# Performance work log

Measured on AMD Instinct MI355X. Metric: run time of the kernel, lower is better.

Reference implementation:

```python
import jax, jax.numpy as jnp
import numpy as np

N_NODES = 100000
N_EDGES = 1600000
D_IN = 64
D_OUT = 64
NUM_ETYPE = 2
NEG_SLOPE = 0.2


def setup_inputs() -> dict:
    key = jax.random.key(0)
    ks = jax.random.split(key, 9)
    feat = jax.random.normal(ks[0], (N_NODES, D_IN), dtype=jnp.float32)
    rel = jax.random.uniform(ks[1], (N_EDGES, NUM_ETYPE), dtype=jnp.float32)
    W_self = jax.random.normal(ks[2], (D_OUT, D_IN), dtype=jnp.float32) * 0.1
    b_self = jax.random.normal(ks[3], (D_OUT,), dtype=jnp.float32) * 0.1
    W_neigh = jax.random.normal(ks[4], (D_OUT, D_IN), dtype=jnp.float32) * 0.1
    b_neigh = jax.random.normal(ks[5], (D_OUT,), dtype=jnp.float32) * 0.1
    attn_e = jax.random.normal(ks[6], (NUM_ETYPE, 1), dtype=jnp.float32)
    src = jax.random.randint(ks[7], (N_EDGES,), 0, N_NODES, dtype=jnp.int32)
    dst = jax.random.randint(ks[8], (N_EDGES,), 0, N_NODES, dtype=jnp.int32)
    return {"feat": feat, "rel": rel, "W_self": W_self, "b_self": b_self,
            "W_neigh": W_neigh, "b_neigh": b_neigh, "attn_e": attn_e,
            "src": src, "dst": dst}


def reference(feat, rel, W_self, b_self, W_neigh, b_neigh, attn_e, src, dst):
    n = feat.shape[0]
    # per-edge attention score: [E, num_etype] @ [num_etype, 1] -> [E]
    e = jnp.squeeze(rel @ attn_e, axis=1)
    e = jax.nn.leaky_relu(e, negative_slope=NEG_SLOPE)
    # edge_softmax: segment softmax over edges grouped by destination node
    emax = jax.ops.segment_max(e, dst, num_segments=n)          # [N]
    ex = jnp.exp(e - emax[dst])                                  # [E]
    denom = jax.ops.segment_sum(ex, dst, num_segments=n)        # [N]
    a = ex / denom[dst]                                          # [E]
    # u_mul_e + sum aggregation: neigh[v] = sum_e a_e * feat[src_e]
    m = feat[src] * a[:, None]                                   # [E, D_IN]
    h_neigh = jax.ops.segment_sum(m, dst, num_segments=n)       # [N, D_IN]
    # rst = fc_self(h_self) + fc_neigh(h_neigh)  (torch Linear: x @ W.T + b)
    return feat @ W_self.T + b_self + h_neigh @ W_neigh.T + b_neigh
```

## Files before the change

kernel.cpp:

```cpp
#include <hip/hip_runtime.h>
#include <hip/hip_bf16.h>

#define N_NODES 100000
#define N_EDGES 1600000
#define D 64
#define NEG_SLOPE 0.2f

#define BSHIFT 10
#define BNODES 1024
#define NBUCK ((N_NODES + BNODES - 1) >> BSHIFT)
#define BUCKET_CAP 17408
#define P1_EPB 4096
#define P1_T 512
#define P1_IT (P1_EPB / P1_T)

__global__ __launch_bounds__(P1_T) void binning_kernel(
    const float2* __restrict__ rel, const float* __restrict__ attn_e,
    const int* __restrict__ src, const int* __restrict__ dst,
    int* __restrict__ bucket_cursor, uint2* __restrict__ binned)
{
    __shared__ uint2 staged1[P1_EPB];
    __shared__ uint2 staged2[P1_EPB];
    __shared__ int cnt[NBUCK];
    __shared__ int excl[NBUCK];
    __shared__ int chunkbase[NBUCK];

    int tid = threadIdx.x;
    int e0 = blockIdx.x * P1_EPB;
    int n = min(P1_EPB, N_EDGES - e0);

    for (int b = tid; b < NBUCK; b += P1_T) cnt[b] = 0;
    __syncthreads();

    float a0 = attn_e[0], a1 = attn_e[1];

    int myslot[P1_IT];
    #pragma unroll
    for (int j = 0; j < P1_IT; ++j) {
        int i = tid + j * P1_T;
        if (i < n) {
            int e = e0 + i;
            float2 r = rel[e];
            float sc = r.x * a0 + r.y * a1;
            sc = (sc > 0.f) ? sc : NEG_SLOPE * sc;
            float ev = __expf(sc);
            unsigned u = __float_as_uint(ev) + 0x8000u;
            unsigned wcode = (u >> 16) & 0x7FFFu;
            unsigned s = (unsigned)src[e];
            unsigned d = (unsigned)dst[e];
            staged1[i] = make_uint2((s << 15) | wcode, d);
            myslot[j] = atomicAdd(&cnt[d >> BSHIFT], 1);
        }
    }
    __syncthreads();
    if (tid == 0) {
        int run = 0;
        for (int b = 0; b < NBUCK; ++b) { excl[b] = run; run += cnt[b]; }
    }
    __syncthreads();
    #pragma unroll
    for (int j = 0; j < P1_IT; ++j) {
        int i = tid + j * P1_T;
        if (i < n) {
            uint2 v = staged1[i];
            staged2[excl[v.y >> BSHIFT] + myslot[j]] = v;
        }
    }
    if (tid < NBUCK)
        chunkbase[tid] = atomicAdd(&bucket_cursor[tid], cnt[tid]);
    __syncthreads();
    for (int i = tid; i < n; i += P1_T) {
        uint2 v = staged2[i];
        int b = (int)(v.y >> BSHIFT);
        binned[(size_t)b * BUCKET_CAP + chunkbase[b] + (i - excl[b])] = v;
    }
}

__global__ __launch_bounds__(1024) void csr_kernel(
    const int* __restrict__ bucket_cursor, const uint2* __restrict__ binned,
    int* __restrict__ offsets, unsigned* __restrict__ edata)
{
    __shared__ unsigned vals[BUCKET_CAP];
    __shared__ int hist[BNODES];
    __shared__ int nexcl[BNODES];
    __shared__ int cur[BNODES];
    __shared__ int bc[NBUCK];
    __shared__ int base_sh;

    int b = blockIdx.x;
    int tid = threadIdx.x;

    if (tid < NBUCK) bc[tid] = bucket_cursor[tid];
    hist[tid] = 0;
    cur[tid] = 0;
    __syncthreads();
    if (tid == 0) {
        int s = 0;
        for (int i = 0; i < b; ++i) s += bc[i];
        base_sh = s;
    }
    __syncthreads();
    int count = bc[b];
    int base = base_sh;
    const uint2* bin = binned + (size_t)b * BUCKET_CAP;

    for (int i = tid; i < count; i += 1024)
        atomicAdd(&hist[bin[i].y & (BNODES - 1)], 1);
    __syncthreads();

    int h = hist[tid];
    nexcl[tid] = h;
    __syncthreads();
    for (int d = 1; d < BNODES; d <<= 1) {
        int u = (tid >= d) ? nexcl[tid - d] : 0;
        __syncthreads();
        nexcl[tid] += u;
        __syncthreads();
    }
    int excl = nexcl[tid] - h;
    __syncthreads();
    nexcl[tid] = excl;
    __syncthreads();

    int node = (b << BSHIFT) + tid;
    if (node < N_NODES) offsets[node] = base + excl;
    if (b == NBUCK - 1 && tid == 0) offsets[N_NODES] = N_EDGES;

    for (int i = tid; i < count; i += 1024) {
        uint2 e = bin[i];
        int d = e.y & (BNODES - 1);
        int t = atomicAdd(&cur[d], 1);
        vals[nexcl[d] + t] = e.x;
    }
    __syncthreads();
    for (int i = tid; i < count; i += 1024)
        edata[base + i] = vals[i];
}

__global__ __launch_bounds__(512) void gemm_fused_kernel(
    const float* __restrict__ feat, const float* __restrict__ W_self,
    const float* __restrict__ W_neigh, const float* __restrict__ b_self,
    const float* __restrict__ b_neigh, float* __restrict__ out,
    __hip_bfloat16* __restrict__ g)
{
    __shared__ float Wt[2][D][D + 1];
    __shared__ float fs[64 * D];
    int tid = threadIdx.x;
    #pragma unroll
    for (int i = 0; i < 8; ++i) {
        int idx = tid + i * 512;
        Wt[0][idx & 63][idx >> 6] = W_self[idx];
        Wt[1][idx & 63][idx >> 6] = W_neigh[idx];
    }
    {
        long base4 = (long)blockIdx.x * 1024;
        const float4* f4 = (const float4*)feat;
        float4* s4 = (float4*)fs;
        #pragma unroll
        for (int i = 0; i < 2; ++i) {
            int idx = tid + i * 512;
            if (base4 + idx < (long)N_NODES * D / 4) s4[idx] = f4[base4 + idx];
        }
    }
    __syncthreads();

    int lane = tid & 63;
    int wave = tid >> 6;
    int m = wave >> 2;
    int sw = wave & 3;
    float w[D];
    #pragma unroll
    for (int k = 0; k < D; ++k) w[k] = Wt[m][k][lane];
    float bias = (m == 0) ? (b_self[lane] + b_neigh[lane]) : 0.f;

    int r0 = blockIdx.x * 64 + sw * 16;
    #pragma unroll 1
    for (int rr = 0; rr < 16; ++rr) {
        int r = r0 + rr;
        if (r >= N_NODES) break;
        const float4* frow = (const float4*)(fs + (sw * 16 + rr) * D);
        float acc = 0.f;
        #pragma unroll
        for (int k4 = 0; k4 < 16; ++k4) {
            float4 f = frow[k4];
            acc += f.x * w[4*k4]   + f.y * w[4*k4+1]
                 + f.z * w[4*k4+2] + f.w * w[4*k4+3];
        }
        if (m == 0) out[(size_t)r * D + lane] = acc + bias;
        else        g[(size_t)r * D + lane] = __float2bfloat16(acc);
    }
}

__global__ __launch_bounds__(256) void aggregate_kernel(
    const uint* __restrict__ g32, const unsigned* __restrict__ edata,
    const int* __restrict__ offsets, float* __restrict__ out)
{
    int v = blockIdx.x * 4 + (threadIdx.x >> 6);
    int lane = threadIdx.x & 63;
    int q = lane >> 4;
    int t = lane & 15;
    int lo = offsets[v], hi = offsets[v + 1];
    float4 acc = make_float4(0.f, 0.f, 0.f, 0.f);
    float sum = 0.f;

    for (int i = lo; i < hi; i += 8) {
        int e0 = i + q;
        int e1 = i + 4 + q;
        int ec0 = (e0 < hi) ? e0 : hi - 1;
        int ec1 = (e1 < hi) ? e1 : hi - 1;
        unsigned p0 = edata[ec0];
        unsigned p1 = edata[ec1];
        float w0 = (e0 < hi) ? __uint_as_float((p0 & 0x7FFFu) << 16) : 0.f;
        float w1 = (e1 < hi) ? __uint_as_float((p1 & 0x7FFFu) << 16) : 0.f;
        const uint2* r0 = (const uint2*)(g32 + (size_t)(p0 >> 15) * (D / 2));
        const uint2* r1 = (const uint2*)(g32 + (size_t)(p1 >> 15) * (D / 2));
        uint2 u0 = r0[t];
        uint2 u1 = r1[t];
        acc.x += w0 * __uint_as_float(u0.x << 16);
        acc.y += w0 * __uint_as_float(u0.x & 0xFFFF0000u);
        acc.z += w0 * __uint_as_float(u0.y << 16);
        acc.w += w0 * __uint_as_float(u0.y & 0xFFFF0000u);
        sum += w0;
        acc.x += w1 * __uint_as_float(u1.x << 16);
        acc.y += w1 * __uint_as_float(u1.x & 0xFFFF0000u);
        acc.z += w1 * __uint_as_float(u1.y << 16);
        acc.w += w1 * __uint_as_float(u1.y & 0xFFFF0000u);
        sum += w1;
    }
    #pragma unroll
    for (int mm = 16; mm <= 32; mm <<= 1) {
        acc.x += __shfl_xor(acc.x, mm, 64);
        acc.y += __shfl_xor(acc.y, mm, 64);
        acc.z += __shfl_xor(acc.z, mm, 64);
        acc.w += __shfl_xor(acc.w, mm, 64);
        sum   += __shfl_xor(sum,   mm, 64);
    }
    if (hi > lo && q == 0) {
        float inv = 1.f / sum;
        float4* orow = (float4*)(out + (size_t)v * D);
        float4 c = orow[t];
        c.x += acc.x * inv; c.y += acc.y * inv;
        c.z += acc.z * inv; c.w += acc.w * inv;
        orow[t] = c;
    }
}

extern "C" void kernel_launch(void* const* d_in, const int* in_sizes, int n_in,
                              void* d_out, int out_size, void* d_ws, size_t ws_size,
                              hipStream_t stream) {
    const float* feat    = (const float*)d_in[0];
    const float* rel     = (const float*)d_in[1];
    const float* W_self  = (const float*)d_in[2];
    const float* b_self  = (const float*)d_in[3];
    const float* W_neigh = (const float*)d_in[4];
    const float* b_neigh = (const float*)d_in[5];
    const float* attn_e  = (const float*)d_in[6];
    const int*   src     = (const int*)d_in[7];
    const int*   dst     = (const int*)d_in[8];
    float* out = (float*)d_out;

    uint2* binned = (uint2*)d_ws;
    __hip_bfloat16* g = (__hip_bfloat16*)(binned + (size_t)NBUCK * BUCKET_CAP);
    unsigned* edata = (unsigned*)((char*)g + (size_t)N_NODES * D * 2);
    int* offsets = (int*)(edata + N_EDGES);
    int* bucket_cursor = offsets + N_NODES + 1;

    hipMemsetAsync(bucket_cursor, 0, NBUCK * sizeof(int), stream);

    binning_kernel<<<(N_EDGES + P1_EPB - 1) / P1_EPB, P1_T, 0, stream>>>(
        (const float2*)rel, attn_e, src, dst, bucket_cursor, binned);
    csr_kernel<<<NBUCK, 1024, 0, stream>>>(
        bucket_cursor, binned, offsets, edata);
    gemm_fused_kernel<<<(N_NODES + 63) / 64, 512, 0, stream>>>(
        feat, W_self, W_neigh, b_self, b_neigh, out, g);
    aggregate_kernel<<<N_NODES / 4, 256, 0, stream>>>(
        (const uint*)g, edata, offsets, out);
}
```

Measured before the change: 217.6 us.

## Shrink CSR buckets to 256 nodes, parallelize scans, load GEMM weights directly

Buckets drop from 1024 to 256 nodes each, giving about 391 buckets. The CSR stage therefore gets roughly four times as many blocks, each with 512 threads and smaller shared-memory tiles, which should raise occupancy. The serial single-thread prefix sums over bucket counts in binning and CSR become parallel Hillis-Steele scans, removing a serial bottleneck that now grows with bucket count. The GEMM kernel reads weight rows straight from global memory as float4 instead of transposing them through shared memory, and sets launch bounds to two blocks per CU. The trade-offs are more global atomics and scattered writes per binning block, and a bucket capacity that leaves less headroom for skewed destination distributions.

```diff
diff --git a/kernel.cpp b/kernel.cpp
--- a/kernel.cpp
+++ b/kernel.cpp
@@ -6,10 +6,10 @@
 #define D 64
 #define NEG_SLOPE 0.2f
 
-#define BSHIFT 10
-#define BNODES 1024
+#define BSHIFT 8
+#define BNODES 256
 #define NBUCK ((N_NODES + BNODES - 1) >> BSHIFT)
-#define BUCKET_CAP 17408
+#define BUCKET_CAP 4672
 #define P1_EPB 4096
 #define P1_T 512
 #define P1_IT (P1_EPB / P1_T)
@@ -24,6 +24,7 @@
     __shared__ int cnt[NBUCK];
     __shared__ int excl[NBUCK];
     __shared__ int chunkbase[NBUCK];
+    __shared__ int scanbuf[P1_T];
 
     int tid = threadIdx.x;
     int e0 = blockIdx.x * P1_EPB;
@@ -53,9 +54,17 @@
         }
     }
     __syncthreads();
-    if (tid == 0) {
-        int run = 0;
-        for (int b = 0; b < NBUCK; ++b) { excl[b] = run; run += cnt[b]; }
+    {
+        int c = (tid < NBUCK) ? cnt[tid] : 0;
+        scanbuf[tid] = c;
+        __syncthreads();
+        for (int d = 1; d < P1_T; d <<= 1) {
+            int u = (tid >= d) ? scanbuf[tid - d] : 0;
+            __syncthreads();
+            scanbuf[tid] += u;
+            __syncthreads();
+        }
+        if (tid < NBUCK) excl[tid] = scanbuf[tid] - c;
     }
     __syncthreads();
     #pragma unroll
@@ -76,7 +85,7 @@
     }
 }
 
-__global__ __launch_bounds__(1024) void csr_kernel(
+__global__ __launch_bounds__(512) void csr_kernel(
     const int* __restrict__ bucket_cursor, const uint2* __restrict__ binned,
     int* __restrict__ offsets, unsigned* __restrict__ edata)
 {
@@ -84,74 +93,64 @@
     __shared__ int hist[BNODES];
     __shared__ int nexcl[BNODES];
     __shared__ int cur[BNODES];
-    __shared__ int bc[NBUCK];
-    __shared__ int base_sh;
+    __shared__ int scanbuf[512];
 
     int b = blockIdx.x;
     int tid = threadIdx.x;
 
-    if (tid < NBUCK) bc[tid] = bucket_cursor[tid];
-    hist[tid] = 0;
-    cur[tid] = 0;
-    __syncthreads();
-    if (tid == 0) {
-        int s = 0;
-        for (int i = 0; i < b; ++i) s += bc[i];
-        base_sh = s;
-    }
-    __syncthreads();
-    int count = bc[b];
-    int base = base_sh;
+    if (tid < BNODES) { hist[tid] = 0; cur[tid] = 0; }
+    int c = (tid < NBUCK) ? bucket_cursor[tid] : 0;
+    scanbuf[tid] = c;
+    __syncthreads();
+    for (int d = 1; d < 512; d <<= 1) {
+        int u = (tid >= d) ? scanbuf[tid - d] : 0;
+        __syncthreads();
+        scanbuf[tid] += u;
+        __syncthreads();
+    }
+    int base = (b == 0) ? 0 : scanbuf[b - 1];
+    int count = scanbuf[b] - base;
     const uint2* bin = binned + (size_t)b * BUCKET_CAP;
 
-    for (int i = tid; i < count; i += 1024)
+    for (int i = tid; i < count; i += 512)
         atomicAdd(&hist[bin[i].y & (BNODES - 1)], 1);
     __syncthreads();
 
-    int h = hist[tid];
-    nexcl[tid] = h;
+    int h = (tid < BNODES) ? hist[tid] : 0;
+    scanbuf[tid] = (tid < BNODES) ? h : 0;
     __syncthreads();
     for (int d = 1; d < BNODES; d <<= 1) {
-        int u = (tid >= d) ? nexcl[tid - d] : 0;
-        __syncthreads();
-        nexcl[tid] += u;
-        __syncthreads();
-    }
-    int excl = nexcl[tid] - h;
-    __syncthreads();
-    nexcl[tid] = excl;
+        int u = (tid >= d) ? scanbuf[tid - d] : 0;
+        __syncthreads();
+        scanbuf[tid] += u;
+        __syncthreads();
+    }
+    if (tid < BNODES) nexcl[tid] = scanbuf[tid] - h;
     __syncthreads();
 
     int node = (b << BSHIFT) + tid;
-    if (node < N_NODES) offsets[node] = base + excl;
+    if (tid < BNODES && node < N_NODES) offsets[node] = base + nexcl[tid];
     if (b == NBUCK - 1 && tid == 0) offsets[N_NODES] = N_EDGES;
 
-    for (int i = tid; i < count; i += 1024) {
+    for (int i = tid; i < count; i += 512) {
         uint2 e = bin[i];
         int d = e.y & (BNODES - 1);
         int t = atomicAdd(&cur[d], 1);
         vals[nexcl[d] + t] = e.x;
     }
     __syncthreads();
-    for (int i = tid; i < count; i += 1024)
+    for (int i = tid; i < count; i += 512)
         edata[base + i] = vals[i];
 }
 
-__global__ __launch_bounds__(512) void gemm_fused_kernel(
+__global__ __launch_bounds__(512, 2) void gemm_fused_kernel(
     const float* __restrict__ feat, const float* __restrict__ W_self,
     const float* __restrict__ W_neigh, const float* __restrict__ b_self,
     const float* __restrict__ b_neigh, float* __restrict__ out,
     __hip_bfloat16* __restrict__ g)
 {
-    __shared__ float Wt[2][D][D + 1];
     __shared__ float fs[64 * D];
     int tid = threadIdx.x;
-    #pragma unroll
-    for (int i = 0; i < 8; ++i) {
-        int idx = tid + i * 512;
-        Wt[0][idx & 63][idx >> 6] = W_self[idx];
-        Wt[1][idx & 63][idx >> 6] = W_neigh[idx];
-    }
     {
         long base4 = (long)blockIdx.x * 1024;
         const float4* f4 = (const float4*)feat;
@@ -162,16 +161,18 @@
             if (base4 + idx < (long)N_NODES * D / 4) s4[idx] = f4[base4 + idx];
         }
     }
-    __syncthreads();
 
     int lane = tid & 63;
     int wave = tid >> 6;
     int m = wave >> 2;
     int sw = wave & 3;
-    float w[D];
-    #pragma unroll
-    for (int k = 0; k < D; ++k) w[k] = Wt[m][k][lane];
+    const float4* Wrow = (const float4*)(((m == 0) ? W_self : W_neigh)
+                                         + (size_t)lane * D);
+    float4 w4[16];
+    #pragma unroll
+    for (int k4 = 0; k4 < 16; ++k4) w4[k4] = Wrow[k4];
     float bias = (m == 0) ? (b_self[lane] + b_neigh[lane]) : 0.f;
+    __syncthreads();
 
     int r0 = blockIdx.x * 64 + sw * 16;
     #pragma unroll 1
@@ -183,8 +184,8 @@
         #pragma unroll
         for (int k4 = 0; k4 < 16; ++k4) {
             float4 f = frow[k4];
-            acc += f.x * w[4*k4]   + f.y * w[4*k4+1]
-                 + f.z * w[4*k4+2] + f.w * w[4*k4+3];
+            acc += f.x * w4[k4].x + f.y * w4[k4].y
+                 + f.z * w4[k4].z + f.w * w4[k4].w;
         }
         if (m == 0) out[(size_t)r * D + lane] = acc + bias;
         else        g[(size_t)r * D + lane] = __float2bfloat16(acc);
@@ -269,7 +270,7 @@
 
     binning_kernel<<<(N_EDGES + P1_EPB - 1) / P1_EPB, P1_T, 0, stream>>>(
         (const float2*)rel, attn_e, src, dst, bucket_cursor, binned);
-    csr_kernel<<<NBUCK, 1024, 0, stream>>>(
+    csr_kernel<<<NBUCK, 512, 0, stream>>>(
         bucket_cursor, binned, offsets, edata);
     gemm_fused_kernel<<<(N_NODES + 63) / 64, 512, 0, stream>>>(
         feat, W_self, W_neigh, b_self, b_neigh, out, g);
```

New measurement: 219.6 us. No clear change (+0.9%).
